# Performance work log

Hardware: AMD Instinct MI355X
Metric: run time of the kernel (lower is better)

The kernel has to match this reference:

```python
import jax, jax.numpy as jnp
import numpy as np

N, MA, F, NF = 512, 64, 128, 16
UPDATE_RATIO = 0.1
DECAY = 1.0
EPS = 1e-12  # avoids NaN grad of sqrt at self-distance 0 (torch diagonal is masked out by exp anyway)


def setup_inputs() -> dict:
    key = jax.random.key(0)
    ks = jax.random.split(key, 8)
    z = jax.random.randint(ks[0], (N, MA), 0, 10, dtype=jnp.int64) if jax.config.jax_enable_x64 else jax.random.randint(ks[0], (N, MA), 0, 10, dtype=jnp.int32)
    # pad last few atoms of each molecule with -1 to exercise the mask
    z = z.at[:, MA - 8:].set(-1)
    r = jax.random.normal(ks[1], (N, MA, 3), dtype=jnp.float32) * 3.0
    h = jax.random.normal(ks[2], (N, MA, F), dtype=jnp.float32)
    distances = jnp.linspace(0.5, 6.0, NF, dtype=jnp.float32)
    widths = jax.random.uniform(ks[3], (NF,), dtype=jnp.float32) * 0.5 + 0.5  # keep sigma > 0
    din = F * (1 + NF)  # 2176
    W1 = jax.random.normal(ks[4], (din, 512), dtype=jnp.float32) * (1.0 / np.sqrt(din))
    b1 = jnp.zeros((512,), dtype=jnp.float32)
    W2 = jax.random.normal(ks[5], (512, F), dtype=jnp.float32) * (1.0 / np.sqrt(512.0))
    b2 = jnp.zeros((F,), dtype=jnp.float32)
    return {"z": z, "r": r, "h": h, "distances": distances, "widths": widths,
            "W1": W1, "b1": b1, "W2": W2, "b2": b2}


def reference(z, r, h, distances, widths, W1, b1, W2, b2):
    n, ma = z.shape
    nf = distances.shape[0]
    # pairwise distance: (n, ma, ma)
    dv = r[:, :, None, :] - r[:, None, :, :]
    d = jnp.sqrt(jnp.sum(dv * dv, axis=-1) + EPS)
    mu = distances.reshape(1, nf, 1, 1)
    sigma = widths.reshape(1, nf, 1, 1)
    mask1 = (z > -1).astype(h.dtype)                      # (n, ma)
    pair_mask = mask1[:, :, None] * mask1[:, None, :]     # (n, ma, ma)
    # Gaussian RBF scores, masked: (n, nf, ma, ma)
    w = pair_mask[:, None] * jnp.exp(-((d[:, None] - mu) ** 2) / sigma) * 5.0
    # aggregate neighbor features: (n, ma, nf, F) -> (n, ma, nf*F)
    u = jnp.einsum('nfab,nbc->nafc', w, h).reshape(n, ma, nf * h.shape[-1])
    v = jnp.concatenate([h, u], axis=2)                   # (n, ma, F*(1+nf))
    v = jax.nn.silu(v @ W1 + b1) @ W2 + b2                # MLP 'net'
    h_new = h + v * UPDATE_RATIO * DECAY * mask1[:, :, None]
    return (z, r, h_new)
```

## Files before the change

### kernel.cpp

```cpp
#include <hip/hip_runtime.h>

#define MA 64
#define F 128
#define NF 16
#define HID 512
#define LDUB 144
#define LDWB 144
#define LDT1B 1040
#define UBA 0
#define UBB 18432
#define WLA 36864
#define WLB 55296
#define UBT 9216
#define WLT 9216

typedef float  float4v __attribute__((ext_vector_type(4)));
typedef short  short8  __attribute__((ext_vector_type(8)));
typedef int    int8v   __attribute__((ext_vector_type(8)));

static __device__ __forceinline__ unsigned int pack2bf(float x, float y) {
    unsigned int a = __float_as_uint(x) + 0x8000u;
    unsigned int b = __float_as_uint(y) + 0x8000u;
    return __builtin_amdgcn_perm(b, a, 0x07060302u);
}
static __device__ __forceinline__ unsigned short f2bf1(float x) {
    return (unsigned short)((__float_as_uint(x) + 0x8000u) >> 16);
}
static __device__ __forceinline__ unsigned int pk4fp8(float a, float b, float c, float d) {
    int p = __builtin_amdgcn_cvt_pk_fp8_f32(a, b, 0, false);
    p = __builtin_amdgcn_cvt_pk_fp8_f32(c, d, p, true);
    return (unsigned int)p;
}

#define LGKM_BAR() do {                                        \
    asm volatile("s_waitcnt lgkmcnt(0)" ::: "memory");         \
    __builtin_amdgcn_s_barrier();                              \
    asm volatile("" ::: "memory");                             \
} while (0)

__global__ void pack_frags(const float* __restrict__ W1, const float* __restrict__ W2,
                           unsigned char* __restrict__ w1p, unsigned short* __restrict__ w2p) {
    int gid  = blockIdx.x * 4 + (threadIdx.x >> 6);
    int lane = threadIdx.x & 63;
    int arow = lane & 15;
    int kq   = lane >> 4;
    if (gid < 544) {
        int kt = gid >> 5, jt = gid & 31;
        const float* base = W1 + (size_t)(kt * 128 + kq * 32) * HID + jt * 16 + arow;
        unsigned int o[8];
        #pragma unroll
        for (int p = 0; p < 8; p++)
            o[p] = pk4fp8(base[(p * 4 + 0) * HID], base[(p * 4 + 1) * HID],
                          base[(p * 4 + 2) * HID], base[(p * 4 + 3) * HID]);
        unsigned char* dst = w1p + ((size_t)gid * 64 + lane) * 32;
        *(uint4*)dst        = (uint4){o[0], o[1], o[2], o[3]};
        *(uint4*)(dst + 16) = (uint4){o[4], o[5], o[6], o[7]};
    } else if (gid < 544 + 128) {
        int g2 = gid - 544;
        int kt = g2 >> 3, mt = g2 & 7;
        const float* base = W2 + (size_t)(kt * 32 + kq * 8) * F + mt * 16 + arow;
        short8 o;
        #pragma unroll
        for (int j = 0; j < 8; j++) o[j] = (short)f2bf1(base[j * F]);
        *(short8*)(w2p + ((size_t)g2 * 64 + lane) * 8) = o;
    }
}

__launch_bounds__(1024, 4)
__global__ void node_conv_mfma(const int* __restrict__ z, const float* __restrict__ rr,
        const float* __restrict__ h, const float* __restrict__ dist,
        const float* __restrict__ wid, const float* __restrict__ b1,
        const float* __restrict__ b2,
        const unsigned char* __restrict__ w1p, const unsigned short* __restrict__ w2p,
        float* __restrict__ out) {
    const int n = blockIdx.x;
    const int tid = threadIdx.x;
    const int lane = tid & 63;
    const int wave = tid >> 6;
    const int arow = lane & 15;
    const int quad = lane >> 4;
    const int kgrp = quad * 8;
    const int whi = wave >> 1;
    const int wlo = wave & 1;

    __shared__ __attribute__((aligned(16))) unsigned char lds[73728];
    __shared__ float r_lds[MA][5];

    const int N = gridDim.x;
    const float* hg = h + (size_t)n * MA * F;

    if (tid < MA) {
        int zi = z[n * MA + tid];
        out[(size_t)n * MA + tid] = (float)zi;
        r_lds[tid][0] = rr[(n * MA + tid) * 3 + 0];
        r_lds[tid][1] = rr[(n * MA + tid) * 3 + 1];
        r_lds[tid][2] = rr[(n * MA + tid) * 3 + 2];
        r_lds[tid][3] = (zi > -1) ? 1.0f : 0.0f;
    }
    if (tid < MA * 3)
        out[(size_t)N * MA + (size_t)n * MA * 3 + tid] = rr[(size_t)n * MA * 3 + tid];

    for (int i = tid; i < MA * F / 4; i += 1024) {
        float4 v = ((const float4*)hg)[i];
        int a = i >> 5, c4 = (i & 31) * 4;
        *(unsigned int*)&lds[UBA + a * LDUB + c4] = pk4fp8(v.x, v.y, v.z, v.w);
    }
    short8 ah[2];
    {
        int c = whi * 16 + arow;
        #pragma unroll
        for (int ks2 = 0; ks2 < 2; ks2++)
            #pragma unroll
            for (int j = 0; j < 8; j++)
                ah[ks2][j] = (short)f2bf1(hg[(size_t)(ks2 * 32 + kgrp + j) * F + c]);
    }
    int8v p0, p1, q0, q1;
    {
        const unsigned char* pp = w1p + ((size_t)((wave * 2) * 64 + lane)) * 32;
        p0 = *(const int8v*)pp;
        p1 = *(const int8v*)(pp + 2048);
    }
    __syncthreads();

    const int wa = tid >> 4;
    const int wb0 = (tid & 15) * 4;
    float dpre[4];
    {
        float ax = r_lds[wa][0], ay = r_lds[wa][1], az = r_lds[wa][2];
        float am = r_lds[wa][3];
        #pragma unroll
        for (int j = 0; j < 4; j++) {
            float dx = ax - r_lds[wb0 + j][0];
            float dy = ay - r_lds[wb0 + j][1];
            float dz = az - r_lds[wb0 + j][2];
            float d = sqrtf(dx * dx + dy * dy + dz * dz + 1e-12f);
            float mm = am * r_lds[wb0 + j][3];
            dpre[j] = d + (1.0f - mm) * 1e4f;
        }
    }

    auto EXPW = [&](int fidx, int wlOff) {
        float mu = dist[fidx];
        float isg = 1.0f / wid[fidx];
        float e[4];
        #pragma unroll
        for (int j = 0; j < 4; j++) {
            float t = dpre[j] - mu;
            e[j] = 5.0f * __expf(-t * t * isg);
        }
        uint2 wp = { pack2bf(e[0], e[1]), pack2bf(e[2], e[3]) };
        *(uint2*)&lds[wlOff + wa * LDWB + wb0 * 2] = wp;
    };
    const float4v zf = {0.f, 0.f, 0.f, 0.f};
    auto UG = [&](int wlOff, int ubOff) {
        float4v ud0 = zf, ud1 = zf;
        #pragma unroll
        for (int ks2 = 0; ks2 < 2; ks2++) {
            short8 bw0 = *(const short8*)&lds[wlOff + ((wlo * 2 + 0) * 16 + arow) * LDWB + (ks2 * 32 + kgrp) * 2];
            ud0 = __builtin_amdgcn_mfma_f32_16x16x32_bf16(ah[ks2], bw0, ud0, 0, 0, 0);
            short8 bw1 = *(const short8*)&lds[wlOff + ((wlo * 2 + 1) * 16 + arow) * LDWB + (ks2 * 32 + kgrp) * 2];
            ud1 = __builtin_amdgcn_mfma_f32_16x16x32_bf16(ah[ks2], bw1, ud1, 0, 0, 0);
        }
        unsigned int u0 = pk4fp8(ud0[0], ud0[1], ud0[2], ud0[3]);
        unsigned int u1 = pk4fp8(ud1[0], ud1[1], ud1[2], ud1[3]);
        *(unsigned int*)&lds[ubOff + ((wlo * 2 + 0) * 16 + arow) * LDUB + whi * 16 + quad * 4] = u0;
        *(unsigned int*)&lds[ubOff + ((wlo * 2 + 1) * 16 + arow) * LDUB + whi * 16 + quad * 4] = u1;
    };

    EXPW(0, WLB);
    EXPW(1, WLA);
    EXPW(2, WLA + WLT);
    LGKM_BAR();
    UG(WLB, UBA + UBT);
    LGKM_BAR();

    float4v acc[2][4];
    #pragma unroll
    for (int i = 0; i < 2; i++)
        #pragma unroll
        for (int jv = 0; jv < 4; jv++) acc[i][jv] = zf;

    for (int i = 0; i < 8; i++) {
        const int sel = i & 1;
        const int ubR = sel ? UBB : UBA;
        const int ubW = sel ? UBA : UBB;
        const int wlR = sel ? WLB : WLA;
        const int wlW = sel ? WLA : WLB;

        {
            const unsigned char* pq = w1p + ((size_t)(((2 * i + 1) * 32 + wave * 2) * 64 + lane)) * 32;
            q0 = *(const int8v*)pq;
            q1 = *(const int8v*)(pq + 2048);
        }
        #pragma unroll
        for (int at = 0; at < 4; at++) {
            int8v bfr = *(const int8v*)&lds[ubR + (at * 16 + arow) * LDUB + quad * 32];
            acc[0][at] = __builtin_amdgcn_mfma_scale_f32_16x16x128_f8f6f4(
                p0, bfr, acc[0][at], 0, 0, 0, 127, 0, 127);
            acc[1][at] = __builtin_amdgcn_mfma_scale_f32_16x16x128_f8f6f4(
                p1, bfr, acc[1][at], 0, 0, 0, 127, 0, 127);
        }
        #pragma unroll
        for (int at = 0; at < 4; at++) {
            int8v bfr = *(const int8v*)&lds[ubR + UBT + (at * 16 + arow) * LDUB + quad * 32];
            acc[0][at] = __builtin_amdgcn_mfma_scale_f32_16x16x128_f8f6f4(
                q0, bfr, acc[0][at], 0, 0, 0, 127, 0, 127);
            acc[1][at] = __builtin_amdgcn_mfma_scale_f32_16x16x128_f8f6f4(
                q1, bfr, acc[1][at], 0, 0, 0, 127, 0, 127);
        }
        {
            const unsigned char* pp = w1p + ((size_t)(((2 * i + 2) * 32 + wave * 2) * 64 + lane)) * 32;
            p0 = *(const int8v*)pp;
            p1 = *(const int8v*)(pp + 2048);
        }

        UG(wlR, ubW);
        if (2 * i + 2 <= NF - 1) UG(wlR + WLT, ubW + UBT);
        if (2 * i + 3 <= NF - 1) EXPW(2 * i + 3, wlW);
        if (2 * i + 4 <= NF - 1) EXPW(2 * i + 4, wlW + WLT);

        LGKM_BAR();
    }

    #pragma unroll
    for (int at = 0; at < 4; at++) {
        int8v bfr = *(const int8v*)&lds[UBA + (at * 16 + arow) * LDUB + quad * 32];
        acc[0][at] = __builtin_amdgcn_mfma_scale_f32_16x16x128_f8f6f4(
            p0, bfr, acc[0][at], 0, 0, 0, 127, 0, 127);
        acc[1][at] = __builtin_amdgcn_mfma_scale_f32_16x16x128_f8f6f4(
            p1, bfr, acc[1][at], 0, 0, 0, 127, 0, 127);
    }
    LGKM_BAR();

    float4 b1v[2];
    #pragma unroll
    for (int mt = 0; mt < 2; mt++)
        b1v[mt] = *(const float4*)&b1[wave * 32 + mt * 16 + quad * 4];

    #pragma unroll
    for (int mt = 0; mt < 2; mt++) {
        #pragma unroll
        for (int at = 0; at < 4; at++) {
            float xs[4];
            #pragma unroll
            for (int r = 0; r < 4; r++) {
                float x = acc[mt][at][r] + ((const float*)&b1v[mt])[r];
                xs[r] = x / (1.0f + __expf(-x));
            }
            uint2 pv = { pack2bf(xs[0], xs[1]), pack2bf(xs[2], xs[3]) };
            *(uint2*)&lds[(at * 16 + arow) * LDT1B + (wave * 32 + mt * 16 + quad * 4) * 2] = pv;
        }
    }
    LGKM_BAR();

    float4v g2[2] = { zf, zf };

    short8 awA = *(const short8*)(w2p + ((size_t)(whi) * 64 + lane) * 8);
    #pragma unroll
    for (int ks2 = 0; ks2 < 8; ks2++) {
        const int k1 = 2 * ks2 + 1;
        short8 awB = *(const short8*)(w2p + ((size_t)(k1 * 8 + whi) * 64 + lane) * 8);
        #pragma unroll
        for (int j = 0; j < 2; j++) {
            short8 bt = *(const short8*)&lds[((wlo * 2 + j) * 16 + arow) * LDT1B + ((2 * ks2) * 32 + kgrp) * 2];
            g2[j] = __builtin_amdgcn_mfma_f32_16x16x32_bf16(awA, bt, g2[j], 0, 0, 0);
        }
        const int k2 = (ks2 < 7) ? 2 * ks2 + 2 : 0;
        awA = *(const short8*)(w2p + ((size_t)(k2 * 8 + whi) * 64 + lane) * 8);
        #pragma unroll
        for (int j = 0; j < 2; j++) {
            short8 bt = *(const short8*)&lds[((wlo * 2 + j) * 16 + arow) * LDT1B + ((2 * ks2 + 1) * 32 + kgrp) * 2];
            g2[j] = __builtin_amdgcn_mfma_f32_16x16x32_bf16(awB, bt, g2[j], 0, 0, 0);
        }
    }

    float* outh = out + (size_t)N * MA * 4 + (size_t)n * MA * F;
    const int c0 = whi * 16 + quad * 4;
    float4 b2v = *(const float4*)&b2[c0];
    #pragma unroll
    for (int j = 0; j < 2; j++) {
        int a = (wlo * 2 + j) * 16 + arow;
        float m = r_lds[a][3] * 0.1f;
        float4 hv = *(const float4*)&hg[a * F + c0];
        float4 res;
        res.x = hv.x + (g2[j][0] + b2v.x) * m;
        res.y = hv.y + (g2[j][1] + b2v.y) * m;
        res.z = hv.z + (g2[j][2] + b2v.z) * m;
        res.w = hv.w + (g2[j][3] + b2v.w) * m;
        *(float4*)&outh[(size_t)a * F + c0] = res;
    }
}

extern "C" void kernel_launch(void* const* d_in, const int* in_sizes, int n_in,
                              void* d_out, int out_size, void* d_ws, size_t ws_size,
                              hipStream_t stream) {
    const int*   z    = (const int*)d_in[0];
    const float* rr   = (const float*)d_in[1];
    const float* h    = (const float*)d_in[2];
    const float* dist = (const float*)d_in[3];
    const float* wid  = (const float*)d_in[4];
    const float* W1   = (const float*)d_in[5];
    const float* b1   = (const float*)d_in[6];
    const float* W2   = (const float*)d_in[7];
    const float* b2   = (const float*)d_in[8];
    float* out = (float*)d_out;

    int Nmol = in_sizes[0] / MA;

    unsigned char*  w1p = (unsigned char*)d_ws;
    unsigned short* w2p = (unsigned short*)(w1p + (size_t)544 * 64 * 32);

    pack_frags<<<168, 256, 0, stream>>>(W1, W2, w1p, w2p);
    node_conv_mfma<<<Nmol, 1024, 0, stream>>>(z, rr, h, dist, wid, b1, b2, w1p, w2p, out);
}
```

Measured before the change: 146.5 us.

## Stage all filter slabs in LDS with XOR swizzle, then run the W1 GEMM separately

The old interleaved schedule, which double-buffered two filter slabs of U while overlapping the RBF/UG production with the W1 MFMA loop, is replaced by two phases. The first phase computes all 16 fp8 U slabs into LDS. The second phase runs a simple loop over 17 slabs that feeds the fp8 scaled MFMAs. U is stored unpadded with an XOR swizzle to avoid bank conflicts, which raises LDS use to about 154 KB. This larger footprint limits the kernel to one block per CU and removes the overlap between U generation and the W1 GEMM.

```diff
diff --git a/kernel.cpp b/kernel.cpp
--- a/kernel.cpp
+++ b/kernel.cpp
@@ -4,15 +4,12 @@
 #define F 128
 #define NF 16
 #define HID 512
-#define LDUB 144
+#define SLAB 8192
 #define LDWB 144
 #define LDT1B 1040
-#define UBA 0
-#define UBB 18432
-#define WLA 36864
-#define WLB 55296
-#define UBT 9216
-#define WLT 9216
+#define WL0 139264
+#define WL1 148480
+#define SWZ(row, col) ((((row) * 128) + (col)) ^ (((row) & 7) << 4))
 
 typedef float  float4v __attribute__((ext_vector_type(4)));
 typedef short  short8  __attribute__((ext_vector_type(8)));
@@ -83,7 +80,7 @@
     const int whi = wave >> 1;
     const int wlo = wave & 1;
 
-    __shared__ __attribute__((aligned(16))) unsigned char lds[73728];
+    __shared__ __attribute__((aligned(16))) unsigned char lds[157696];
     __shared__ float r_lds[MA][5];
 
     const int N = gridDim.x;
@@ -103,7 +100,7 @@
     for (int i = tid; i < MA * F / 4; i += 1024) {
         float4 v = ((const float4*)hg)[i];
         int a = i >> 5, c4 = (i & 31) * 4;
-        *(unsigned int*)&lds[UBA + a * LDUB + c4] = pk4fp8(v.x, v.y, v.z, v.w);
+        *(unsigned int*)&lds[SWZ(a, c4)] = pk4fp8(v.x, v.y, v.z, v.w);
     }
     short8 ah[2];
     {
@@ -152,7 +149,7 @@
         *(uint2*)&lds[wlOff + wa * LDWB + wb0 * 2] = wp;
     };
     const float4v zf = {0.f, 0.f, 0.f, 0.f};
-    auto UG = [&](int wlOff, int ubOff) {
+    auto UG = [&](int wlOff, int slabOff) {
         float4v ud0 = zf, ud1 = zf;
         #pragma unroll
         for (int ks2 = 0; ks2 < 2; ks2++) {
@@ -163,16 +160,19 @@
         }
         unsigned int u0 = pk4fp8(ud0[0], ud0[1], ud0[2], ud0[3]);
         unsigned int u1 = pk4fp8(ud1[0], ud1[1], ud1[2], ud1[3]);
-        *(unsigned int*)&lds[ubOff + ((wlo * 2 + 0) * 16 + arow) * LDUB + whi * 16 + quad * 4] = u0;
-        *(unsigned int*)&lds[ubOff + ((wlo * 2 + 1) * 16 + arow) * LDUB + whi * 16 + quad * 4] = u1;
+        *(unsigned int*)&lds[slabOff + SWZ((wlo * 2 + 0) * 16 + arow, whi * 16 + quad * 4)] = u0;
+        *(unsigned int*)&lds[slabOff + SWZ((wlo * 2 + 1) * 16 + arow, whi * 16 + quad * 4)] = u1;
     };
 
-    EXPW(0, WLB);
-    EXPW(1, WLA);
-    EXPW(2, WLA + WLT);
+    EXPW(0, WL0);
     LGKM_BAR();
-    UG(WLB, UBA + UBT);
-    LGKM_BAR();
+    for (int f = 0; f < NF; f++) {
+        const int wlR = (f & 1) ? WL1 : WL0;
+        const int wlW = (f & 1) ? WL0 : WL1;
+        UG(wlR, (f + 1) * SLAB);
+        if (f < NF - 1) EXPW(f + 1, wlW);
+        LGKM_BAR();
+    }
 
     float4v acc[2][4];
     #pragma unroll
@@ -180,55 +180,28 @@
         #pragma unroll
         for (int jv = 0; jv < 4; jv++) acc[i][jv] = zf;
 
-    for (int i = 0; i < 8; i++) {
-        const int sel = i & 1;
-        const int ubR = sel ? UBB : UBA;
-        const int ubW = sel ? UBA : UBB;
-        const int wlR = sel ? WLB : WLA;
-        const int wlW = sel ? WLA : WLB;
-
-        {
-            const unsigned char* pq = w1p + ((size_t)(((2 * i + 1) * 32 + wave * 2) * 64 + lane)) * 32;
+    for (int f = 0; f <= NF; f++) {
+        if (f < NF) {
+            const unsigned char* pq = w1p + ((size_t)(((f + 1) * 32 + wave * 2) * 64 + lane)) * 32;
             q0 = *(const int8v*)pq;
             q1 = *(const int8v*)(pq + 2048);
         }
+        const int sb = f * SLAB;
         #pragma unroll
         for (int at = 0; at < 4; at++) {
-            int8v bfr = *(const int8v*)&lds[ubR + (at * 16 + arow) * LDUB + quad * 32];
+            const int rowb = at * 16 + arow;
+            uint4 lo = *(const uint4*)&lds[sb + SWZ(rowb, quad * 32)];
+            uint4 hi = *(const uint4*)&lds[sb + SWZ(rowb, quad * 32 + 16)];
+            int8v bfr;
+            bfr[0] = (int)lo.x; bfr[1] = (int)lo.y; bfr[2] = (int)lo.z; bfr[3] = (int)lo.w;
+            bfr[4] = (int)hi.x; bfr[5] = (int)hi.y; bfr[6] = (int)hi.z; bfr[7] = (int)hi.w;
             acc[0][at] = __builtin_amdgcn_mfma_scale_f32_16x16x128_f8f6f4(
                 p0, bfr, acc[0][at], 0, 0, 0, 127, 0, 127);
             acc[1][at] = __builtin_amdgcn_mfma_scale_f32_16x16x128_f8f6f4(
                 p1, bfr, acc[1][at], 0, 0, 0, 127, 0, 127);
         }
-        #pragma unroll
-        for (int at = 0; at < 4; at++) {
-            int8v bfr = *(const int8v*)&lds[ubR + UBT + (at * 16 + arow) * LDUB + quad * 32];
-            acc[0][at] = __builtin_amdgcn_mfma_scale_f32_16x16x128_f8f6f4(
-                q0, bfr, acc[0][at], 0, 0, 0, 127, 0, 127);
-            acc[1][at] = __builtin_amdgcn_mfma_scale_f32_16x16x128_f8f6f4(
-                q1, bfr, acc[1][at], 0, 0, 0, 127, 0, 127);
-        }
-        {
-            const unsigned char* pp = w1p + ((size_t)(((2 * i + 2) * 32 + wave * 2) * 64 + lane)) * 32;
-            p0 = *(const int8v*)pp;
-            p1 = *(const int8v*)(pp + 2048);
-        }
-
-        UG(wlR, ubW);
-        if (2 * i + 2 <= NF - 1) UG(wlR + WLT, ubW + UBT);
-        if (2 * i + 3 <= NF - 1) EXPW(2 * i + 3, wlW);
-        if (2 * i + 4 <= NF - 1) EXPW(2 * i + 4, wlW + WLT);
-
-        LGKM_BAR();
-    }
-
-    #pragma unroll
-    for (int at = 0; at < 4; at++) {
-        int8v bfr = *(const int8v*)&lds[UBA + (at * 16 + arow) * LDUB + quad * 32];
-        acc[0][at] = __builtin_amdgcn_mfma_scale_f32_16x16x128_f8f6f4(
-            p0, bfr, acc[0][at], 0, 0, 0, 127, 0, 127);
-        acc[1][at] = __builtin_amdgcn_mfma_scale_f32_16x16x128_f8f6f4(
-            p1, bfr, acc[1][at], 0, 0, 0, 127, 0, 127);
+        p0 = q0;
+        p1 = q1;
     }
     LGKM_BAR();
 
```

Result: slower. 150.1 us (+2.4%).
